# Performance work log

Hardware: AMD Instinct MI355X
Metric: run time of the kernel (lower is better)

Reference implementation:

```python
import jax, jax.numpy as jnp
import numpy as np

N = 100000      # nodes
E = 1600000     # edges (no self-loops; self-loops added in reference, per PyG defaults)
IN = 128        # in_size
HID = 32        # hide_size (per-head channels)
HEADS = 4       # n_heads
OUT = 128       # out_size
NEG_SLOPE = 0.2 # PyG GATConv default negative_slope


def setup_inputs() -> dict:
    key = jax.random.key(0)
    ks = jax.random.split(key, 8)
    x = jax.random.normal(ks[0], (N, IN), jnp.float32)
    # edges guaranteed non-self-loop: dst = (src + offset) % N with offset in [1, N)
    src = jax.random.randint(ks[1], (E,), 0, N, dtype=jnp.int32)
    off = jax.random.randint(ks[2], (E,), 1, N, dtype=jnp.int32)
    dst = ((src + off) % N).astype(jnp.int32)
    edge_index = jnp.stack([src, dst])  # [2, E]
    edge_weight = jax.random.uniform(ks[3], (E,), jnp.float32)
    glorot = lambda k, shape, fan: jax.random.normal(k, shape, jnp.float32) / np.sqrt(fan).astype(np.float32)
    W_gat = glorot(ks[4], (IN, HEADS * HID), IN)      # GATConv lin weight (bias=False)
    att_src = glorot(ks[5], (HEADS, HID), HID)        # GATConv att_src
    att_dst = glorot(ks[6], (HEADS, HID), HID)        # GATConv att_dst
    W_gcn = glorot(ks[7], (HEADS * HID, OUT), HEADS * HID)  # GCNConv weight (bias=False)
    return {"x": x, "edge_index": edge_index, "edge_weight": edge_weight,
            "W_gat": W_gat, "att_src": att_src, "att_dst": att_dst, "W_gcn": W_gcn}


def reference(x, edge_index, edge_weight, W_gat, att_src, att_dst, W_gcn):
    n = x.shape[0]
    loop = jnp.arange(n, dtype=edge_index.dtype)
    src = jnp.concatenate([edge_index[0], loop])  # add self-loops (PyG default)
    dst = jnp.concatenate([edge_index[1], loop])

    # ---- GATConv (concat heads, bias=False) ----
    xp = (x @ W_gat).reshape(n, HEADS, HID)                  # [N,H,C]
    a_s = jnp.einsum('nhc,hc->nh', xp, att_src)              # [N,H]
    a_d = jnp.einsum('nhc,hc->nh', xp, att_dst)
    alpha = jax.nn.leaky_relu(a_s[src] + a_d[dst], NEG_SLOPE)  # [E+N,H]
    m = jax.ops.segment_max(alpha, dst, num_segments=n)     # segment softmax over incoming edges
    e = jnp.exp(alpha - m[dst])
    denom = jax.ops.segment_sum(e, dst, num_segments=n)
    a = e / denom[dst]                                       # [E+N,H]
    y_gat = jax.ops.segment_sum(xp[src] * a[:, :, None], dst, num_segments=n)
    y_gat = y_gat.reshape(n, HEADS * HID)                    # [N, H*C]

    # ---- GCNConv (normalize=True, bias=False), self-loop weight = 1 ----
    ew = jnp.concatenate([edge_weight, jnp.ones((n,), edge_weight.dtype)])
    deg = jax.ops.segment_sum(ew, dst, num_segments=n)
    dinv = jnp.where(deg > 0, jax.lax.rsqrt(deg), 0.0)
    norm = dinv[src] * ew * dinv[dst]                        # [E+N]
    h = y_gat @ W_gcn                                        # [N, OUT]
    out = jax.ops.segment_sum(h[src] * norm[:, None], dst, num_segments=n)
    return out
```

## Files before the change

### kernel.cpp

```cpp
#include <hip/hip_runtime.h>

#define NN 100000
#define EE 1600000
#define TOT (EE + NN)
#define NEG 0.2f
#define NB 256
#define CH 391
#define TILE 4096
#define NTILES ((EE + TILE - 1) / TILE)
#define GEMM_BLKS ((NN + 63) / 64)
#define LDA 132

typedef unsigned int uint;
typedef unsigned short ushort;

#define BLO(u) __uint_as_float((u) << 16)
#define BHI(u) __uint_as_float((u) & 0xffff0000u)

__device__ inline ushort f2bf(float f) {
    uint u = __float_as_uint(f);
    return (ushort)((u + 0x7fff + ((u >> 16) & 1)) >> 16);
}

__device__ inline int imin(int a, int b) { return a < b ? a : b; }


__launch_bounds__(256) __global__
void k_bcount(const int* __restrict__ dst, int* __restrict__ bcnt) {
    __shared__ int h[NB];
    int t = threadIdx.x;
    h[t] = 0;
    __syncthreads();
    int base = blockIdx.x * TILE;
#pragma unroll
    for (int r = 0; r < 16; ++r) {
        int e = base + r * 256 + t;
        if (e < EE) atomicAdd(&h[dst[e] / CH], 1);
    }
    __syncthreads();
    if (h[t]) atomicAdd(&bcnt[t], h[t]);
}


__launch_bounds__(NB) __global__
void k_bprefix(const int* __restrict__ bcnt, int* __restrict__ boff,
               int* __restrict__ bcsr, int* __restrict__ bfill) {
    __shared__ int s1[NB], s2[NB];
    int t = threadIdx.x;
    int c = bcnt[t];
    int nb0 = t * CH;
    int nib = imin(nb0 + CH, NN) - nb0;
    s1[t] = c; s2[t] = c + nib;
    __syncthreads();
    for (int off = 1; off < NB; off <<= 1) {
        int a = (t >= off) ? s1[t - off] : 0;
        int b = (t >= off) ? s2[t - off] : 0;
        __syncthreads();
        s1[t] += a; s2[t] += b;
        __syncthreads();
    }
    int ex = s1[t] - c;
    boff[t] = ex;
    bfill[t] = ex;
    bcsr[t] = s2[t] - (c + nib);
    if (t == NB - 1) boff[NB] = EE;
}


__launch_bounds__(256) __global__
void k_bin(const int* __restrict__ src, const int* __restrict__ dst,
           const float* __restrict__ ew, int* __restrict__ bfill,
           long long* __restrict__ binned) {
    __shared__ long long recs[TILE];
    __shared__ ushort    bkt[TILE];
    __shared__ int hist[NB], eoff[NB], gbase[NB];
    int t = threadIdx.x;
    hist[t] = 0;
    __syncthreads();
    int base = blockIdx.x * TILE;
    int cnt = imin(TILE, EE - base);
    long long rec[16]; int binfo[16];
#pragma unroll
    for (int r = 0; r < 16; ++r) {
        int i = r * 256 + t;
        if (i < cnt) {
            int e = base + i;
            int s = src[e], d = dst[e];
            float w = ew[e];
            int b = d / CH;
            int ldst = d - b * CH;
            int rk = atomicAdd(&hist[b], 1);
            rec[r] = (long long)(uint)(s | (ldst << 17)) |
                     ((long long)__float_as_uint(w) << 32);
            binfo[r] = b | (rk << 8);
        }
    }
    __syncthreads();
    int c = hist[t];
    eoff[t] = c;
    __syncthreads();
    for (int off = 1; off < NB; off <<= 1) {
        int a = (t >= off) ? eoff[t - off] : 0;
        __syncthreads();
        eoff[t] += a;
        __syncthreads();
    }
    int ex = eoff[t] - c;
    gbase[t] = atomicAdd(&bfill[t], c);
    eoff[t] = ex;
    __syncthreads();
#pragma unroll
    for (int r = 0; r < 16; ++r) {
        int i = r * 256 + t;
        if (i < cnt) {
            int b = binfo[r] & 255, rk = binfo[r] >> 8;
            int slot = eoff[b] + rk;
            recs[slot] = rec[r];
            bkt[slot] = (ushort)b;
        }
    }
    __syncthreads();
#pragma unroll
    for (int r = 0; r < 16; ++r) {
        int i = r * 256 + t;
        if (i < cnt) {
            int b = bkt[i];
            binned[gbase[b] + (i - eoff[b])] = recs[i];
        }
    }
}


__device__ __forceinline__ void gemm1_body(
    int bid, const float* __restrict__ A, const float* __restrict__ W,
    ushort* __restrict__ C16, const float* __restrict__ att_s,
    const float* __restrict__ att_d, float* __restrict__ a_s,
    float* __restrict__ a_d) {
    int lane = threadIdx.x & 63;
    int cg = __builtin_amdgcn_readfirstlane(threadIdx.x >> 6);
    int row = bid * 64 + lane;
    bool valid = row < NN;
    if (!valid) row = NN - 1;
    const float* __restrict__ a = A + (size_t)row * 128;
    const float* __restrict__ w = W + cg * 32;
    float acc[32];
#pragma unroll
    for (int c = 0; c < 32; ++c) acc[c] = 0.f;
    float4 xv = *(const float4*)(a);
    for (int k = 0; k < 128; k += 4) {
        float4 nx = xv;
        if (k < 124) nx = *(const float4*)(a + k + 4);
        float xs[4] = {xv.x, xv.y, xv.z, xv.w};
#pragma unroll
        for (int kk = 0; kk < 4; ++kk) {
            const float* wr = w + (k + kk) * 128;
            float xk = xs[kk];
#pragma unroll
            for (int c = 0; c < 32; ++c) acc[c] = fmaf(xk, wr[c], acc[c]);
        }
        xv = nx;
    }
    if (valid) {
        ushort* o = C16 + (size_t)row * 128 + cg * 32;
#pragma unroll
        for (int c = 0; c < 32; c += 8) {
            uint4 p;
            p.x = (uint)f2bf(acc[c+0]) | ((uint)f2bf(acc[c+1]) << 16);
            p.y = (uint)f2bf(acc[c+2]) | ((uint)f2bf(acc[c+3]) << 16);
            p.z = (uint)f2bf(acc[c+4]) | ((uint)f2bf(acc[c+5]) << 16);
            p.w = (uint)f2bf(acc[c+6]) | ((uint)f2bf(acc[c+7]) << 16);
            *(uint4*)(o + c) = p;
        }
        const float* as = att_s + cg * 32;
        const float* ad = att_d + cg * 32;
        float s0 = 0.f, s1 = 0.f;
#pragma unroll
        for (int c = 0; c < 32; ++c) {
            s0 = fmaf(acc[c], as[c], s0);
            s1 = fmaf(acc[c], ad[c], s1);
        }
        a_s[row * 4 + cg] = s0;
        a_d[row * 4 + cg] = s1;
    }
}


__launch_bounds__(256) __global__
void k_fine_gemm(const long long* __restrict__ binned, const int* __restrict__ boff,
                 const int* __restrict__ bcsr, int* __restrict__ row_off,
                 long long* __restrict__ csr,
                 const float* __restrict__ A, const float* __restrict__ W,
                 ushort* __restrict__ C16, const float* __restrict__ att_s,
                 const float* __restrict__ att_d, float* __restrict__ a_s,
                 float* __restrict__ a_d) {
    if (blockIdx.x >= NB) {
        gemm1_body(blockIdx.x - NB, A, W, C16, att_s, att_d, a_s, a_d);
        return;
    }
    __shared__ int hist[CH];
    __shared__ int excl[CH];
    __shared__ int sc[512];
    int t = threadIdx.x;
    int b = blockIdx.x;
    int e0 = boff[b], e1 = boff[b + 1];
    int nb0 = b * CH;
    int nnode = imin(CH, NN - nb0);
    const int2* __restrict__ bn = (const int2*)binned;
    hist[t] = 0;
    if (t + 256 < CH) hist[t + 256] = 0;
    __syncthreads();
    for (int i = e0 + t; i < e1; i += 256)
        atomicAdd(&hist[bn[i].x >> 17], 1);
    __syncthreads();
    int v0 = (t < nnode) ? hist[t] + 1 : 0;
    int v1 = (t + 256 < nnode) ? hist[t + 256] + 1 : 0;
    sc[t] = v0; sc[t + 256] = v1;
    __syncthreads();
    for (int off = 1; off < 512; off <<= 1) {
        int a0 = (t >= off) ? sc[t - off] : 0;
        int a1 = (t + 256 >= off) ? sc[t + 256 - off] : 0;
        __syncthreads();
        sc[t] += a0; sc[t + 256] += a1;
        __syncthreads();
    }
    int csr0 = bcsr[b];
    if (t < nnode) {
        excl[t] = csr0 + sc[t] - v0;
        row_off[nb0 + t] = excl[t];
    }
    if (t + 256 < nnode) {
        excl[t + 256] = csr0 + sc[t + 256] - v1;
        row_off[nb0 + t + 256] = excl[t + 256];
    }
    if (b == 0 && t == 0) row_off[NN] = TOT;
    hist[t] = 0;
    if (t + 256 < CH) hist[t + 256] = 0;
    __syncthreads();
    for (int i = e0 + t; i < e1; i += 256) {
        int2 r = bn[i];
        int ld = r.x >> 17;
        int rk = atomicAdd(&hist[ld], 1);
        long long rec = (long long)(uint)(r.x & 0x1FFFF) |
                        ((long long)(uint)r.y << 32);
        csr[excl[ld] + rk] = rec;
    }
    __syncthreads();
    for (int i = t; i < nnode; i += 256) {
        int n = nb0 + i;
        csr[excl[i] + hist[i]] = (long long)(uint)n | (0x3F800000LL << 32);
    }
}


__launch_bounds__(512) __global__
void k_gat_g2(const int* __restrict__ row_off, const int2* __restrict__ csr,
              const float* __restrict__ a_s, const float* __restrict__ a_d,
              const ushort* __restrict__ xp16, const float* __restrict__ W,
              ushort* __restrict__ h16, float* __restrict__ dinv) {
    __shared__ float As[64 * LDA];
    __shared__ float sdinv[64];
    int lane = threadIdx.x & 63;
    int wv = threadIdx.x >> 6;
    int grp = lane >> 4, sl = lane & 15, h2 = sl >> 2;
    int nbase = blockIdx.x * 64;

    for (int rnd = 0; rnd < 8; ++rnd) {
        int r = (rnd << 3) | wv;
        int node = nbase + r;
        if (node < NN) {
            int base = row_off[node], end = row_off[node + 1];
            float adh = a_d[node * 4 + h2];
            float acc[8];
#pragma unroll
            for (int j = 0; j < 8; ++j) acc[j] = 0.f;
            float den = 0.f, wsum = 0.f;
            int na = end - 1;
            int i0 = base + grp;
            int2 e0v = csr[imin(i0,      na)];
            int2 e1v = csr[imin(i0 + 4,  na)];
            int2 e2v = csr[imin(i0 + 8,  na)];
            int2 e3v = csr[imin(i0 + 12, na)];
            for (int i = i0; i < end; i += 16) {
                int2 p0 = csr[imin(i + 16, na)];
                int2 p1 = csr[imin(i + 20, na)];
                int2 p2 = csr[imin(i + 24, na)];
                int2 p3 = csr[imin(i + 28, na)];
                uint4 q0 = *(const uint4*)(xp16 + (size_t)e0v.x * 128 + sl * 8);
                uint4 q1 = *(const uint4*)(xp16 + (size_t)e1v.x * 128 + sl * 8);
                uint4 q2 = *(const uint4*)(xp16 + (size_t)e2v.x * 128 + sl * 8);
                uint4 q3 = *(const uint4*)(xp16 + (size_t)e3v.x * 128 + sl * 8);
                float al0 = a_s[e0v.x * 4 + h2] + adh;
                float al1 = a_s[e1v.x * 4 + h2] + adh;
                float al2 = a_s[e2v.x * 4 + h2] + adh;
                float al3 = a_s[e3v.x * 4 + h2] + adh;
                al0 = al0 > 0.f ? al0 : NEG * al0;
                al1 = al1 > 0.f ? al1 : NEG * al1;
                al2 = al2 > 0.f ? al2 : NEG * al2;
                al3 = al3 > 0.f ? al3 : NEG * al3;
                float aw0 = __expf(al0);
                float aw1 = (i + 4  < end) ? __expf(al1) : 0.f;
                float aw2 = (i + 8  < end) ? __expf(al2) : 0.f;
                float aw3 = (i + 12 < end) ? __expf(al3) : 0.f;
                float w0 = __int_as_float(e0v.y);
                float w1 = (i + 4  < end) ? __int_as_float(e1v.y) : 0.f;
                float w2 = (i + 8  < end) ? __int_as_float(e2v.y) : 0.f;
                float w3 = (i + 12 < end) ? __int_as_float(e3v.y) : 0.f;
                den  += (aw0 + aw1) + (aw2 + aw3);
                wsum += (w0 + w1) + (w2 + w3);
                acc[0] = fmaf(aw0, BLO(q0.x), fmaf(aw1, BLO(q1.x), fmaf(aw2, BLO(q2.x), fmaf(aw3, BLO(q3.x), acc[0]))));
                acc[1] = fmaf(aw0, BHI(q0.x), fmaf(aw1, BHI(q1.x), fmaf(aw2, BHI(q2.x), fmaf(aw3, BHI(q3.x), acc[1]))));
                acc[2] = fmaf(aw0, BLO(q0.y), fmaf(aw1, BLO(q1.y), fmaf(aw2, BLO(q2.y), fmaf(aw3, BLO(q3.y), acc[2]))));
                acc[3] = fmaf(aw0, BHI(q0.y), fmaf(aw1, BHI(q1.y), fmaf(aw2, BHI(q2.y), fmaf(aw3, BHI(q3.y), acc[3]))));
                acc[4] = fmaf(aw0, BLO(q0.z), fmaf(aw1, BLO(q1.z), fmaf(aw2, BLO(q2.z), fmaf(aw3, BLO(q3.z), acc[4]))));
                acc[5] = fmaf(aw0, BHI(q0.z), fmaf(aw1, BHI(q1.z), fmaf(aw2, BHI(q2.z), fmaf(aw3, BHI(q3.z), acc[5]))));
                acc[6] = fmaf(aw0, BLO(q0.w), fmaf(aw1, BLO(q1.w), fmaf(aw2, BLO(q2.w), fmaf(aw3, BLO(q3.w), acc[6]))));
                acc[7] = fmaf(aw0, BHI(q0.w), fmaf(aw1, BHI(q1.w), fmaf(aw2, BHI(q2.w), fmaf(aw3, BHI(q3.w), acc[7]))));
                e0v = p0; e1v = p1; e2v = p2; e3v = p3;
            }
#pragma unroll
            for (int j = 0; j < 8; ++j) {
                acc[j] += __shfl_xor(acc[j], 16);
                acc[j] += __shfl_xor(acc[j], 32);
            }
            den  += __shfl_xor(den, 16);   den  += __shfl_xor(den, 32);
            wsum += __shfl_xor(wsum, 16);  wsum += __shfl_xor(wsum, 32);
            if (grp == 0) {
                float il = 1.f / den;
                float* o = &As[r * LDA + sl * 8];
                *(float4*)(o)     = make_float4(acc[0]*il, acc[1]*il, acc[2]*il, acc[3]*il);
                *(float4*)(o + 4) = make_float4(acc[4]*il, acc[5]*il, acc[6]*il, acc[7]*il);
                if (sl == 0) {
                    float dv = rsqrtf(wsum);
                    sdinv[r] = dv;
                    dinv[node] = dv;
                }
            }
        } else if (grp == 0) {
            float* o = &As[r * LDA + sl * 8];
            *(float4*)(o)     = make_float4(0.f, 0.f, 0.f, 0.f);
            *(float4*)(o + 4) = make_float4(0.f, 0.f, 0.f, 0.f);
            if (sl == 0) sdinv[r] = 0.f;
        }
    }
    __syncthreads();

    int cg = __builtin_amdgcn_readfirstlane(wv);
    int row = nbase + lane;
    bool valid = row < NN;
    const float* __restrict__ w = W + cg * 16;
    const float* __restrict__ a = &As[lane * LDA];
    float acc[16];
#pragma unroll
    for (int c = 0; c < 16; ++c) acc[c] = 0.f;
    for (int k = 0; k < 128; k += 4) {
        float4 xv = *(const float4*)(a + k);
        float xs[4] = {xv.x, xv.y, xv.z, xv.w};
#pragma unroll
        for (int kk = 0; kk < 4; ++kk) {
            const float* wr = w + (k + kk) * 128;
            float xk = xs[kk];
#pragma unroll
            for (int c = 0; c < 16; ++c) acc[c] = fmaf(xk, wr[c], acc[c]);
        }
    }
    if (valid) {
        float sc = sdinv[lane];
        ushort* o = h16 + (size_t)row * 128 + cg * 16;
#pragma unroll
        for (int c = 0; c < 16; c += 8) {
            uint4 p;
            p.x = (uint)f2bf(acc[c+0]*sc) | ((uint)f2bf(acc[c+1]*sc) << 16);
            p.y = (uint)f2bf(acc[c+2]*sc) | ((uint)f2bf(acc[c+3]*sc) << 16);
            p.z = (uint)f2bf(acc[c+4]*sc) | ((uint)f2bf(acc[c+5]*sc) << 16);
            p.w = (uint)f2bf(acc[c+6]*sc) | ((uint)f2bf(acc[c+7]*sc) << 16);
            *(uint4*)(o + c) = p;
        }
    }
}


__launch_bounds__(256) __global__
void k_gcn(const int* __restrict__ row_off, const int2* __restrict__ csr,
           const float* __restrict__ dinv, const ushort* __restrict__ h16,
           float* __restrict__ out) {
    int lane = threadIdx.x & 63;
    int node = blockIdx.x * 4 + (threadIdx.x >> 6);
    int base = row_off[node], end = row_off[node + 1];
    float dn = dinv[node];
    int grp = lane >> 4, sl = lane & 15;
    float acc[8];
#pragma unroll
    for (int j = 0; j < 8; ++j) acc[j] = 0.f;
    int na = end - 1;
    int i0 = base + grp;
    int2 e0v = csr[imin(i0,      na)];
    int2 e1v = csr[imin(i0 + 4,  na)];
    int2 e2v = csr[imin(i0 + 8,  na)];
    int2 e3v = csr[imin(i0 + 12, na)];
    for (int i = i0; i < end; i += 16) {
        int2 p0 = csr[imin(i + 16, na)];
        int2 p1 = csr[imin(i + 20, na)];
        int2 p2 = csr[imin(i + 24, na)];
        int2 p3 = csr[imin(i + 28, na)];
        uint4 q0 = *(const uint4*)(h16 + (size_t)e0v.x * 128 + sl * 8);
        uint4 q1 = *(const uint4*)(h16 + (size_t)e1v.x * 128 + sl * 8);
        uint4 q2 = *(const uint4*)(h16 + (size_t)e2v.x * 128 + sl * 8);
        uint4 q3 = *(const uint4*)(h16 + (size_t)e3v.x * 128 + sl * 8);
        float c0 = __int_as_float(e0v.y) * dn;
        float c1 = (i + 4  < end) ? __int_as_float(e1v.y) * dn : 0.f;
        float c2 = (i + 8  < end) ? __int_as_float(e2v.y) * dn : 0.f;
        float c3 = (i + 12 < end) ? __int_as_float(e3v.y) * dn : 0.f;
        acc[0] = fmaf(c0, BLO(q0.x), fmaf(c1, BLO(q1.x), fmaf(c2, BLO(q2.x), fmaf(c3, BLO(q3.x), acc[0]))));
        acc[1] = fmaf(c0, BHI(q0.x), fmaf(c1, BHI(q1.x), fmaf(c2, BHI(q2.x), fmaf(c3, BHI(q3.x), acc[1]))));
        acc[2] = fmaf(c0, BLO(q0.y), fmaf(c1, BLO(q1.y), fmaf(c2, BLO(q2.y), fmaf(c3, BLO(q3.y), acc[2]))));
        acc[3] = fmaf(c0, BHI(q0.y), fmaf(c1, BHI(q1.y), fmaf(c2, BHI(q2.y), fmaf(c3, BHI(q3.y), acc[3]))));
        acc[4] = fmaf(c0, BLO(q0.z), fmaf(c1, BLO(q1.z), fmaf(c2, BLO(q2.z), fmaf(c3, BLO(q3.z), acc[4]))));
        acc[5] = fmaf(c0, BHI(q0.z), fmaf(c1, BHI(q1.z), fmaf(c2, BHI(q2.z), fmaf(c3, BHI(q3.z), acc[5]))));
        acc[6] = fmaf(c0, BLO(q0.w), fmaf(c1, BLO(q1.w), fmaf(c2, BLO(q2.w), fmaf(c3, BLO(q3.w), acc[6]))));
        acc[7] = fmaf(c0, BHI(q0.w), fmaf(c1, BHI(q1.w), fmaf(c2, BHI(q2.w), fmaf(c3, BHI(q3.w), acc[7]))));
        e0v = p0; e1v = p1; e2v = p2; e3v = p3;
    }
#pragma unroll
    for (int j = 0; j < 8; ++j) {
        acc[j] += __shfl_xor(acc[j], 16);
        acc[j] += __shfl_xor(acc[j], 32);
    }
    if (grp == 0) {
        float* o = out + (size_t)node * 128 + sl * 8;
        *(float4*)(o)     = make_float4(acc[0], acc[1], acc[2], acc[3]);
        *(float4*)(o + 4) = make_float4(acc[4], acc[5], acc[6], acc[7]);
    }
}


extern "C" void kernel_launch(void* const* d_in, const int* in_sizes, int n_in,
                              void* d_out, int out_size, void* d_ws, size_t ws_size,
                              hipStream_t stream) {
    const float* x    = (const float*)d_in[0];
    const int*   ei   = (const int*)  d_in[1];
    const float* ew   = (const float*)d_in[2];
    const float* Wg   = (const float*)d_in[3];
    const float* atts = (const float*)d_in[4];
    const float* attd = (const float*)d_in[5];
    const float* Wc   = (const float*)d_in[6];
    float* out = (float*)d_out;

    float* a_s   = (float*)d_ws;
    float* a_d   = a_s + 400000;
    float* dinvp = a_d + 400000;
    int* row_off = (int*)(dinvp + 100000);
    int* bcnt    = row_off + 100004;
    int* boff    = bcnt + NB;
    int* bcsr    = boff + NB + 1;
    int* bfill   = bcsr + NB;
    long long* csr = (long long*)(bfill + NB + 1);
    ushort* xp16 = (ushort*)(csr + 1700000);
    ushort* h16  = xp16 + 12800000;
    long long* binned = (long long*)h16;

    const int* srcv = ei;
    const int* dstv = ei + EE;

    hipMemsetAsync(bcnt, 0, NB * sizeof(int), stream);
    k_bcount <<<NTILES, 256, 0, stream>>>(dstv, bcnt);
    k_bprefix<<<1, NB, 0, stream>>>(bcnt, boff, bcsr, bfill);
    k_bin    <<<NTILES, 256, 0, stream>>>(srcv, dstv, ew, bfill, binned);
    k_fine_gemm<<<NB + GEMM_BLKS, 256, 0, stream>>>(
        binned, boff, bcsr, row_off, csr,
        x, Wg, xp16, atts, attd, a_s, a_d);
    k_gat_g2<<<GEMM_BLKS, 512, 0, stream>>>(row_off, (const int2*)csr, a_s, a_d,
                                            xp16, Wc, h16, dinvp);
    k_gcn  <<<NN / 4, 256, 0, stream>>>(row_off, (const int2*)csr, dinvp, h16, out);
}
```

Before: 452.3 us.

## Register-tile both dense GEMMs with shared-memory A rows and per-lane column pairs

Both dense matmuls (x@W_gat fused with the attention dot products, and the GCN projection in the GAT kernel) change from one-row-per-lane with 32 or 16 columns per thread to a register tile of 8 rows by 2 columns per lane. Rows are staged in shared memory and each lane loads a float2 of W per k. This gives coalesced W reads and broadcast LDS reads of A. The first GEMM now uses 32-row blocks with a shared buffer that is also reused by the histogram path. The attention scores are reduced across 16 lanes with shuffles. Trade-offs are more blocks, more LDS traffic per FMA, and the loss of tail handling in the first GEMM, which relies on NN being divisible by 32.

```diff
diff --git a/kernel.cpp b/kernel.cpp
--- a/kernel.cpp
+++ b/kernel.cpp
@@ -8,7 +8,8 @@
 #define CH 391
 #define TILE 4096
 #define NTILES ((EE + TILE - 1) / TILE)
-#define GEMM_BLKS ((NN + 63) / 64)
+#define GAT_BLKS ((NN + 63) / 64)
+#define GEMM1_BLKS (NN / 32)
 #define LDA 132
 
 typedef unsigned int uint;
@@ -135,52 +136,51 @@
     int bid, const float* __restrict__ A, const float* __restrict__ W,
     ushort* __restrict__ C16, const float* __restrict__ att_s,
     const float* __restrict__ att_d, float* __restrict__ a_s,
-    float* __restrict__ a_d) {
-    int lane = threadIdx.x & 63;
-    int cg = __builtin_amdgcn_readfirstlane(threadIdx.x >> 6);
-    int row = bid * 64 + lane;
-    bool valid = row < NN;
-    if (!valid) row = NN - 1;
-    const float* __restrict__ a = A + (size_t)row * 128;
-    const float* __restrict__ w = W + cg * 32;
-    float acc[32];
-#pragma unroll
-    for (int c = 0; c < 32; ++c) acc[c] = 0.f;
-    float4 xv = *(const float4*)(a);
+    float* __restrict__ a_d, float* __restrict__ At) {
+    int t = threadIdx.x;
+    int lane = t & 63, wv = t >> 6;
+    int rbase = bid * 32;
+    const float4* Ag = (const float4*)(A + (size_t)rbase * 128);
+    float4* At4 = (float4*)At;
+#pragma unroll
+    for (int i = 0; i < 4; ++i) At4[i * 256 + t] = Ag[i * 256 + t];
+    __syncthreads();
+    int r0 = wv * 8;
+    int c0 = lane * 2;
+    const float* wp = W + c0;
+    float acc[8][2];
+#pragma unroll
+    for (int r = 0; r < 8; ++r) { acc[r][0] = 0.f; acc[r][1] = 0.f; }
     for (int k = 0; k < 128; k += 4) {
-        float4 nx = xv;
-        if (k < 124) nx = *(const float4*)(a + k + 4);
-        float xs[4] = {xv.x, xv.y, xv.z, xv.w};
-#pragma unroll
-        for (int kk = 0; kk < 4; ++kk) {
-            const float* wr = w + (k + kk) * 128;
-            float xk = xs[kk];
-#pragma unroll
-            for (int c = 0; c < 32; ++c) acc[c] = fmaf(xk, wr[c], acc[c]);
-        }
-        xv = nx;
-    }
-    if (valid) {
-        ushort* o = C16 + (size_t)row * 128 + cg * 32;
-#pragma unroll
-        for (int c = 0; c < 32; c += 8) {
-            uint4 p;
-            p.x = (uint)f2bf(acc[c+0]) | ((uint)f2bf(acc[c+1]) << 16);
-            p.y = (uint)f2bf(acc[c+2]) | ((uint)f2bf(acc[c+3]) << 16);
-            p.z = (uint)f2bf(acc[c+4]) | ((uint)f2bf(acc[c+5]) << 16);
-            p.w = (uint)f2bf(acc[c+6]) | ((uint)f2bf(acc[c+7]) << 16);
-            *(uint4*)(o + c) = p;
-        }
-        const float* as = att_s + cg * 32;
-        const float* ad = att_d + cg * 32;
-        float s0 = 0.f, s1 = 0.f;
-#pragma unroll
-        for (int c = 0; c < 32; ++c) {
-            s0 = fmaf(acc[c], as[c], s0);
-            s1 = fmaf(acc[c], ad[c], s1);
-        }
-        a_s[row * 4 + cg] = s0;
-        a_d[row * 4 + cg] = s1;
+        float2 w0 = *(const float2*)(wp + (k + 0) * 128);
+        float2 w1 = *(const float2*)(wp + (k + 1) * 128);
+        float2 w2 = *(const float2*)(wp + (k + 2) * 128);
+        float2 w3 = *(const float2*)(wp + (k + 3) * 128);
+#pragma unroll
+        for (int r = 0; r < 8; ++r) {
+            float4 av = *(const float4*)(At + (r0 + r) * 128 + k);
+            acc[r][0] = fmaf(av.w, w3.x, fmaf(av.z, w2.x, fmaf(av.y, w1.x, fmaf(av.x, w0.x, acc[r][0]))));
+            acc[r][1] = fmaf(av.w, w3.y, fmaf(av.z, w2.y, fmaf(av.y, w1.y, fmaf(av.x, w0.y, acc[r][1]))));
+        }
+    }
+    float as0 = att_s[c0], as1 = att_s[c0 + 1];
+    float ad0 = att_d[c0], ad1 = att_d[c0 + 1];
+    int head = lane >> 4;
+#pragma unroll
+    for (int r = 0; r < 8; ++r) {
+        int row = rbase + r0 + r;
+        uint pv = (uint)f2bf(acc[r][0]) | ((uint)f2bf(acc[r][1]) << 16);
+        *(uint*)(C16 + (size_t)row * 128 + c0) = pv;
+        float s0 = fmaf(acc[r][1], as1, acc[r][0] * as0);
+        float s1 = fmaf(acc[r][1], ad1, acc[r][0] * ad0);
+        s0 += __shfl_xor(s0, 1); s0 += __shfl_xor(s0, 2);
+        s0 += __shfl_xor(s0, 4); s0 += __shfl_xor(s0, 8);
+        s1 += __shfl_xor(s1, 1); s1 += __shfl_xor(s1, 2);
+        s1 += __shfl_xor(s1, 4); s1 += __shfl_xor(s1, 8);
+        if ((lane & 15) == 0) {
+            a_s[row * 4 + head] = s0;
+            a_d[row * 4 + head] = s1;
+        }
     }
 }
 
@@ -193,13 +193,15 @@
                  ushort* __restrict__ C16, const float* __restrict__ att_s,
                  const float* __restrict__ att_d, float* __restrict__ a_s,
                  float* __restrict__ a_d) {
+    __shared__ int smem[4096];
     if (blockIdx.x >= NB) {
-        gemm1_body(blockIdx.x - NB, A, W, C16, att_s, att_d, a_s, a_d);
+        gemm1_body(blockIdx.x - NB, A, W, C16, att_s, att_d, a_s, a_d,
+                   (float*)smem);
         return;
     }
-    __shared__ int hist[CH];
-    __shared__ int excl[CH];
-    __shared__ int sc[512];
+    int* hist = smem;
+    int* excl = smem + 400;
+    int* sc   = smem + 800;
     int t = threadIdx.x;
     int b = blockIdx.x;
     int e0 = boff[b], e1 = boff[b + 1];
@@ -344,36 +346,32 @@
     }
     __syncthreads();
 
-    int cg = __builtin_amdgcn_readfirstlane(wv);
-    int row = nbase + lane;
-    bool valid = row < NN;
-    const float* __restrict__ w = W + cg * 16;
-    const float* __restrict__ a = &As[lane * LDA];
-    float acc[16];
-#pragma unroll
-    for (int c = 0; c < 16; ++c) acc[c] = 0.f;
+    int r0 = wv * 8;
+    int c0 = lane * 2;
+    const float* __restrict__ wp = W + c0;
+    float acc2[8][2];
+#pragma unroll
+    for (int r = 0; r < 8; ++r) { acc2[r][0] = 0.f; acc2[r][1] = 0.f; }
     for (int k = 0; k < 128; k += 4) {
-        float4 xv = *(const float4*)(a + k);
-        float xs[4] = {xv.x, xv.y, xv.z, xv.w};
-#pragma unroll
-        for (int kk = 0; kk < 4; ++kk) {
-            const float* wr = w + (k + kk) * 128;
-            float xk = xs[kk];
-#pragma unroll
-            for (int c = 0; c < 16; ++c) acc[c] = fmaf(xk, wr[c], acc[c]);
-        }
-    }
-    if (valid) {
-        float sc = sdinv[lane];
-        ushort* o = h16 + (size_t)row * 128 + cg * 16;
-#pragma unroll
-        for (int c = 0; c < 16; c += 8) {
-            uint4 p;
-            p.x = (uint)f2bf(acc[c+0]*sc) | ((uint)f2bf(acc[c+1]*sc) << 16);
-            p.y = (uint)f2bf(acc[c+2]*sc) | ((uint)f2bf(acc[c+3]*sc) << 16);
-            p.z = (uint)f2bf(acc[c+4]*sc) | ((uint)f2bf(acc[c+5]*sc) << 16);
-            p.w = (uint)f2bf(acc[c+6]*sc) | ((uint)f2bf(acc[c+7]*sc) << 16);
-            *(uint4*)(o + c) = p;
+        float2 w0 = *(const float2*)(wp + (k + 0) * 128);
+        float2 w1 = *(const float2*)(wp + (k + 1) * 128);
+        float2 w2 = *(const float2*)(wp + (k + 2) * 128);
+        float2 w3 = *(const float2*)(wp + (k + 3) * 128);
+#pragma unroll
+        for (int r = 0; r < 8; ++r) {
+            float4 av = *(const float4*)(&As[(r0 + r) * LDA + k]);
+            acc2[r][0] = fmaf(av.w, w3.x, fmaf(av.z, w2.x, fmaf(av.y, w1.x, fmaf(av.x, w0.x, acc2[r][0]))));
+            acc2[r][1] = fmaf(av.w, w3.y, fmaf(av.z, w2.y, fmaf(av.y, w1.y, fmaf(av.x, w0.y, acc2[r][1]))));
+        }
+    }
+#pragma unroll
+    for (int r = 0; r < 8; ++r) {
+        int row = nbase + r0 + r;
+        if (row < NN) {
+            float sc2 = sdinv[r0 + r];
+            uint pv = (uint)f2bf(acc2[r][0] * sc2) |
+                      ((uint)f2bf(acc2[r][1] * sc2) << 16);
+            *(uint*)(h16 + (size_t)row * 128 + c0) = pv;
         }
     }
 }
@@ -465,10 +463,10 @@
     k_bcount <<<NTILES, 256, 0, stream>>>(dstv, bcnt);
     k_bprefix<<<1, NB, 0, stream>>>(bcnt, boff, bcsr, bfill);
     k_bin    <<<NTILES, 256, 0, stream>>>(srcv, dstv, ew, bfill, binned);
-    k_fine_gemm<<<NB + GEMM_BLKS, 256, 0, stream>>>(
+    k_fine_gemm<<<NB + GEMM1_BLKS, 256, 0, stream>>>(
         binned, boff, bcsr, row_off, csr,
         x, Wg, xp16, atts, attd, a_s, a_d);
-    k_gat_g2<<<GEMM_BLKS, 512, 0, stream>>>(row_off, (const int2*)csr, a_s, a_d,
-                                            xp16, Wc, h16, dinvp);
+    k_gat_g2<<<GAT_BLKS, 512, 0, stream>>>(row_off, (const int2*)csr, a_s, a_d,
+                                           xp16, Wc, h16, dinvp);
     k_gcn  <<<NN / 4, 256, 0, stream>>>(row_off, (const int2*)csr, dinvp, h16, out);
 }
```

After: 446.6 us. Within noise of the previous version (-1.3%).
